# Kernel tuning notes

Measured on AMD Instinct MI355X. Metric: run time of the kernel, lower is better.

Reference implementation:

```python
import jax, jax.numpy as jnp
import numpy as np

SURROGATE_SCALE = 10.0  # SuperSpike-style surrogate slope

@jax.custom_vjp
def spike_fn(v):
    # Heaviside step: spike if membrane minus threshold > 0
    return (v > 0).astype(v.dtype)

def _spike_fwd(v):
    return spike_fn(v), v

def _spike_bwd(v, g):
    # SuperSpike surrogate gradient: 1 / (scale*|v| + 1)^2
    sg = 1.0 / jnp.square(SURROGATE_SCALE * jnp.abs(v) + 1.0)
    return (g * sg,)

spike_fn.defvjp(_spike_fwd, _spike_bwd)


def setup_inputs() -> dict:
    key = jax.random.key(0)
    B, C, T = 64, 256, 2000
    x = jax.random.normal(key, (B, C, T), dtype=jnp.float32)
    alpha = jnp.float32(0.75)
    beta = jnp.float32(0.65)
    Vth = jnp.ones((C,), dtype=jnp.float32)
    return {"x": x, "alpha": alpha, "beta": beta, "Vth": Vth}


def reference(x, alpha, beta, Vth):
    # LIF membrane recurrence over time (neuron_type='LIF', flatten_output=False)
    # x: (B, C, T) -> spk_rec: (B, C, T)
    B, C, T = x.shape
    xs = jnp.transpose(x, (2, 0, 1))  # (T, B, C)

    def step(carry, x_t):
        mem, spk = carry
        rst = spk * Vth                      # einsum('ab,b->ab', spk, Vth)
        mem = (mem - rst) * beta + x_t * alpha  # LIF scales input by alpha
        spk = spike_fn(mem - Vth)
        return (mem, spk), spk

    init = (jnp.zeros((B, C), x.dtype), jnp.zeros((B, C), x.dtype))
    _, spk_rec = jax.lax.scan(step, init, xs)  # (T, B, C)
    return jnp.transpose(spk_rec, (1, 2, 0))   # (B, C, T)
```

## Files before the change

### kernel.cpp

```cpp
#include <hip/hip_runtime.h>


constexpr int T_LEN = 2000;
constexpr int CH    = 32;
constexpr int NQ    = CH / 4;
constexpr int NFULL = 62;
constexpr int TAILQ = (T_LEN - NFULL * CH)/4;
constexpr int LDSW  = 33;

__device__ __forceinline__ void load_tile(float4 (&buf)[NQ], const float4* __restrict__ p) {
#pragma unroll
    for (int q = 0; q < NQ; ++q) buf[q] = p[q];
}

__device__ __forceinline__ void load_tail(float4 (&buf)[NQ], const float4* __restrict__ p) {
#pragma unroll
    for (int q = 0; q < TAILQ; ++q) buf[q] = p[q];
}

__device__ __forceinline__ float lif_step(float xval, float alpha, float beta, float vth,
                                          float& mem, float& vdiff, bool& spk) {
#pragma clang fp contract(off)
    float xa = xval * alpha;
    float p0 = mem   * beta;
    float p1 = vdiff * beta;
    float q0 = p0 + xa;
    float q1 = p1 + xa;
    mem   = spk ? q1 : q0;
    vdiff = mem - vth;
    spk   = vdiff > 0.0f;
    return spk ? 1.0f : 0.0f;
}

template <int N>
__device__ __forceinline__ void compute_tile(const float4 (&buf)[NQ], float* shrow,
                                             float alpha, float beta, float vth,
                                             float& mem, float& vdiff, bool& spk) {
#pragma clang fp contract(off)
#pragma unroll
    for (int q = 0; q < N; ++q) {
        float4 xv = buf[q];
        shrow[q*4 + 0] = lif_step(xv.x, alpha, beta, vth, mem, vdiff, spk);
        shrow[q*4 + 1] = lif_step(xv.y, alpha, beta, vth, mem, vdiff, spk);
        shrow[q*4 + 2] = lif_step(xv.z, alpha, beta, vth, mem, vdiff, spk);
        shrow[q*4 + 3] = lif_step(xv.w, alpha, beta, vth, mem, vdiff, spk);
    }
}

__device__ __forceinline__ void store_tile(const float* __restrict__ sh, int sub, int off,
                                           float* __restrict__ op) {
#pragma unroll
    for (int k = 0; k < 8; ++k) {
        const float* p = sh + (sub + 8*k) * LDSW + off * 4;
        float4 s = make_float4(p[0], p[1], p[2], p[3]);
        *reinterpret_cast<float4*>(op + (size_t)(8*k) * T_LEN) = s;
    }
}

__global__ __launch_bounds__(64) void lif_fwd_kernel(const float* __restrict__ x,
                                                     const float* __restrict__ alpha_p,
                                                     const float* __restrict__ beta_p,
                                                     const float* __restrict__ vth_p,
                                                     float* __restrict__ out,
                                                     int C, int rows) {
#pragma clang fp contract(off)
    __shared__ float sh[64 * LDSW];

    const int lane = threadIdx.x;
    const int row0 = blockIdx.x * 64;
    const int row  = row0 + lane;
    if (row >= rows) return;

    const float alpha = alpha_p[0];
    const float beta  = beta_p[0];
    const float vth   = vth_p[(unsigned)row % (unsigned)C];

    const float4* __restrict__ xq = reinterpret_cast<const float4*>(x + (size_t)row * T_LEN);
    float* __restrict__ shrow = sh + lane * LDSW;
    const int sub = lane >> 3;
    const int off = lane & 7;
    float* __restrict__ outp = out + (size_t)(row0 + sub) * T_LEN + off * 4;

    float mem = 0.0f, vdiff = 0.0f;
    bool  spk = false;
    float4 A[NQ], B[NQ];

    load_tile(A, xq);
    int t = 0;
    for (int i = 0; i < 30; ++i) {
        load_tile(B, xq + (size_t)(t + 1) * NQ);
        __builtin_amdgcn_sched_barrier(0);
        compute_tile<NQ>(A, shrow, alpha, beta, vth, mem, vdiff, spk);
        store_tile(sh, sub, off, outp + (size_t)t * CH);
        ++t;
        load_tile(A, xq + (size_t)(t + 1) * NQ);
        __builtin_amdgcn_sched_barrier(0);
        compute_tile<NQ>(B, shrow, alpha, beta, vth, mem, vdiff, spk);
        store_tile(sh, sub, off, outp + (size_t)t * CH);
        ++t;
    }
    load_tile(B, xq + (size_t)61 * NQ);
    __builtin_amdgcn_sched_barrier(0);
    compute_tile<NQ>(A, shrow, alpha, beta, vth, mem, vdiff, spk);
    store_tile(sh, sub, off, outp + (size_t)60 * CH);

    load_tail(A, xq + (size_t)62 * NQ);
    __builtin_amdgcn_sched_barrier(0);
    compute_tile<NQ>(B, shrow, alpha, beta, vth, mem, vdiff, spk);
    store_tile(sh, sub, off, outp + (size_t)61 * CH);

    compute_tile<TAILQ>(A, shrow, alpha, beta, vth, mem, vdiff, spk);
    {
        const int subt = lane >> 2;
        const int offt = lane & 3;
        float* opt = out + (size_t)(row0 + subt) * T_LEN + NFULL * CH + offt * 4;
#pragma unroll
        for (int k = 0; k < 4; ++k) {
            const float* p = sh + (subt + 16*k) * LDSW + offt * 4;
            float4 s = make_float4(p[0], p[1], p[2], p[3]);
            *reinterpret_cast<float4*>(opt + (size_t)(16*k) * T_LEN) = s;
        }
    }
}

extern "C" void kernel_launch(void* const* d_in, const int* in_sizes, int n_in,
                              void* d_out, int out_size, void* d_ws, size_t ws_size,
                              hipStream_t stream) {
    const float* x     = (const float*)d_in[0];
    const float* alpha = (const float*)d_in[1];
    const float* beta  = (const float*)d_in[2];
    const float* vth   = (const float*)d_in[3];
    float* out = (float*)d_out;

    const int C    = in_sizes[3];
    const int rows = in_sizes[0] / T_LEN;

    dim3 grid((rows + 63) / 64), block(64);
    lif_fwd_kernel<<<grid, block, 0, stream>>>(x, alpha, beta, vth, out, C, rows);
}
```

Before: 250.1 us.

## Stream input tiles via global_load_lds into triple-buffered LDS with vmcnt waits

Input loads no longer go into register double-buffers. They use direct global-to-LDS loads into a three-slot shared ring, and explicit s_waitcnt vmcnt counts manage a two-tile prefetch depth. This is meant to deepen memory latency hiding and cut VGPR pressure for the serial, latency-bound recurrence. It costs extra LDS reads per tile and relies on hand-counted vmcnt values that also include the output stores, so a miscount could cause races or over-waiting.

```diff
diff --git a/kernel.cpp b/kernel.cpp
--- a/kernel.cpp
+++ b/kernel.cpp
@@ -7,15 +7,24 @@
 constexpr int NFULL = 62;
 constexpr int TAILQ = (T_LEN - NFULL * CH)/4;
 constexpr int LDSW  = 33;
+constexpr int XBUF  = NQ * 256;
 
-__device__ __forceinline__ void load_tile(float4 (&buf)[NQ], const float4* __restrict__ p) {
-#pragma unroll
-    for (int q = 0; q < NQ; ++q) buf[q] = p[q];
+typedef float nfloat4 __attribute__((ext_vector_type(4)));
+
+#define WAITV(N) do { \
+    asm volatile("s_waitcnt vmcnt(" #N ")" ::: "memory"); \
+    __builtin_amdgcn_sched_barrier(0); } while (0)
+
+__device__ __forceinline__ void glds16(const float* gp, float* lp) {
+    __builtin_amdgcn_global_load_lds(
+        (const __attribute__((address_space(1))) void*)gp,
+        (__attribute__((address_space(3))) void*)lp, 16, 0, 0);
 }
 
-__device__ __forceinline__ void load_tail(float4 (&buf)[NQ], const float4* __restrict__ p) {
+template <int N>
+__device__ __forceinline__ void load_tile(const float* xlt, float* xb) {
 #pragma unroll
-    for (int q = 0; q < TAILQ; ++q) buf[q] = p[q];
+    for (int q = 0; q < N; ++q) glds16(xlt + q * 4, xb + q * 256);
 }
 
 __device__ __forceinline__ float lif_step(float xval, float alpha, float beta, float vth,
@@ -33,17 +42,23 @@
 }
 
 template <int N>
-__device__ __forceinline__ void compute_tile(const float4 (&buf)[NQ], float* shrow,
-                                             float alpha, float beta, float vth,
-                                             float& mem, float& vdiff, bool& spk) {
+__device__ __forceinline__ void read_x(nfloat4 (&xv)[NQ], const float* xrd) {
+#pragma unroll
+    for (int q = 0; q < N; ++q)
+        xv[q] = *reinterpret_cast<const nfloat4*>(xrd + q * 256);
+}
+
+template <int N>
+__device__ __forceinline__ void lif_tile(const nfloat4 (&xv)[NQ], float* shrow,
+                                         float alpha, float beta, float vth,
+                                         float& mem, float& vdiff, bool& spk) {
 #pragma clang fp contract(off)
 #pragma unroll
     for (int q = 0; q < N; ++q) {
-        float4 xv = buf[q];
-        shrow[q*4 + 0] = lif_step(xv.x, alpha, beta, vth, mem, vdiff, spk);
-        shrow[q*4 + 1] = lif_step(xv.y, alpha, beta, vth, mem, vdiff, spk);
-        shrow[q*4 + 2] = lif_step(xv.z, alpha, beta, vth, mem, vdiff, spk);
-        shrow[q*4 + 3] = lif_step(xv.w, alpha, beta, vth, mem, vdiff, spk);
+        shrow[q*4 + 0] = lif_step(xv[q].x, alpha, beta, vth, mem, vdiff, spk);
+        shrow[q*4 + 1] = lif_step(xv[q].y, alpha, beta, vth, mem, vdiff, spk);
+        shrow[q*4 + 2] = lif_step(xv[q].z, alpha, beta, vth, mem, vdiff, spk);
+        shrow[q*4 + 3] = lif_step(xv[q].w, alpha, beta, vth, mem, vdiff, spk);
     }
 }
 
@@ -64,6 +79,7 @@
                                                      float* __restrict__ out,
                                                      int C, int rows) {
 #pragma clang fp contract(off)
+    __shared__ float shx[3 * XBUF];
     __shared__ float sh[64 * LDSW];
 
     const int lane = threadIdx.x;
@@ -74,8 +90,10 @@
     const float alpha = alpha_p[0];
     const float beta  = beta_p[0];
     const float vth   = vth_p[(unsigned)row % (unsigned)C];
+    asm volatile("" :: "v"(alpha), "v"(beta), "v"(vth));
 
-    const float4* __restrict__ xq = reinterpret_cast<const float4*>(x + (size_t)row * T_LEN);
+    const float* xl  = x + (size_t)row * T_LEN;
+    const float* xrd = shx + lane * 4;
     float* __restrict__ shrow = sh + lane * LDSW;
     const int sub = lane >> 3;
     const int off = lane & 7;
@@ -83,33 +101,41 @@
 
     float mem = 0.0f, vdiff = 0.0f;
     bool  spk = false;
-    float4 A[NQ], B[NQ];
+    nfloat4 xv[NQ];
 
-    load_tile(A, xq);
-    int t = 0;
-    for (int i = 0; i < 30; ++i) {
-        load_tile(B, xq + (size_t)(t + 1) * NQ);
-        __builtin_amdgcn_sched_barrier(0);
-        compute_tile<NQ>(A, shrow, alpha, beta, vth, mem, vdiff, spk);
+    load_tile<NQ>(xl,            shx + 0 * XBUF);
+    load_tile<NQ>(xl + CH,       shx + 1 * XBUF);
+
+    WAITV(8);
+    read_x<NQ>(xv, xrd + 0 * XBUF);
+    load_tile<NQ>(xl + 2 * CH,   shx + 2 * XBUF);
+    lif_tile<NQ>(xv, shrow, alpha, beta, vth, mem, vdiff, spk);
+    store_tile(sh, sub, off, outp);
+
+    int par = 1;
+    for (int t = 1; t <= 59; ++t) {
+        WAITV(16);
+        read_x<NQ>(xv, xrd + par * XBUF);
+        int par2 = par + 2; if (par2 >= 3) par2 -= 3;
+        load_tile<NQ>(xl + (size_t)(t + 2) * CH, shx + par2 * XBUF);
+        lif_tile<NQ>(xv, shrow, alpha, beta, vth, mem, vdiff, spk);
         store_tile(sh, sub, off, outp + (size_t)t * CH);
-        ++t;
-        load_tile(A, xq + (size_t)(t + 1) * NQ);
-        __builtin_amdgcn_sched_barrier(0);
-        compute_tile<NQ>(B, shrow, alpha, beta, vth, mem, vdiff, spk);
-        store_tile(sh, sub, off, outp + (size_t)t * CH);
-        ++t;
+        if (++par == 3) par = 0;
     }
-    load_tile(B, xq + (size_t)61 * NQ);
-    __builtin_amdgcn_sched_barrier(0);
-    compute_tile<NQ>(A, shrow, alpha, beta, vth, mem, vdiff, spk);
+    WAITV(16);
+    read_x<NQ>(xv, xrd + 0 * XBUF);
+    load_tile<TAILQ>(xl + (size_t)62 * CH, shx + 2 * XBUF);
+    lif_tile<NQ>(xv, shrow, alpha, beta, vth, mem, vdiff, spk);
     store_tile(sh, sub, off, outp + (size_t)60 * CH);
 
-    load_tail(A, xq + (size_t)62 * NQ);
-    __builtin_amdgcn_sched_barrier(0);
-    compute_tile<NQ>(B, shrow, alpha, beta, vth, mem, vdiff, spk);
+    WAITV(12);
+    read_x<NQ>(xv, xrd + 1 * XBUF);
+    lif_tile<NQ>(xv, shrow, alpha, beta, vth, mem, vdiff, spk);
     store_tile(sh, sub, off, outp + (size_t)61 * CH);
 
-    compute_tile<TAILQ>(A, shrow, alpha, beta, vth, mem, vdiff, spk);
+    WAITV(8);
+    read_x<TAILQ>(xv, xrd + 2 * XBUF);
+    lif_tile<TAILQ>(xv, shrow, alpha, beta, vth, mem, vdiff, spk);
     {
         const int subt = lane >> 2;
         const int offt = lane & 3;
```

Result: slower. 260.0 us (+4.0%).
